# Optimization experiments

Hardware: AMD Instinct MI355X
Metric: run time of the kernel (lower is better)

Reference implementation:

```python
import jax, jax.numpy as jnp
import numpy as np

E = 512        # embed_dim == AutoNCP output_size (motor neurons)
UNITS = 1024   # ncp_units (inter + command + motor)
B = 64         # batch
T = 1024       # sequence length
LN_EPS = 1e-5
SPARSITY = 0.5  # AutoNCP default sparsity_level


def _ncp_sizes():
    rem = UNITS - E
    n_cmd = max(int(0.4 * rem), 1)
    n_inter = rem - n_cmd
    return n_inter, n_cmd, E


def _fanout_mask(rng, n_src, n_dst, fanout):
    # each source neuron connects to `fanout` random targets (NCP-style wiring)
    m = np.zeros((n_src, n_dst), np.float32)
    idx = np.argsort(rng.random((n_src, n_dst)), axis=1)[:, :fanout]
    m[np.arange(n_src)[:, None], idx] = 1.0
    return m


def setup_inputs() -> dict:
    key = jax.random.key(0)
    rng = np.random.default_rng(22222)
    n_inter, n_cmd, n_motor = _ncp_sizes()
    density = 1.0 - SPARSITY
    sensory_fanout = max(int(n_inter * density), 1)
    inter_fanout = max(int(n_cmd * density), 1)
    motor_fanin = max(int(n_cmd * density), 1)
    m0 = _fanout_mask(rng, E, n_inter, sensory_fanout)        # sensory -> inter
    m1 = _fanout_mask(rng, n_inter, n_cmd, inter_fanout)      # inter -> command
    m2 = _fanout_mask(rng, n_motor, n_cmd, motor_fanin).T     # command -> motor (fanin per motor)

    def full_mask(m_in, h):
        # WiredCfCCell: concat ones for the recurrent (hidden) part, then transpose
        # -> mask shape [h, in + h], matching Linear weight [h, in + h]
        return jnp.asarray(np.concatenate([m_in, np.ones((h, h), np.float32)], axis=0).T)

    masks = [full_mask(m0, n_inter), full_mask(m1, n_cmd), full_mask(m2, n_motor)]
    ins = [E, n_inter, n_cmd]
    hs = [n_inter, n_cmd, n_motor]
    d = {}
    ks = jax.random.split(key, 32)
    ki = 0
    for l in range(3):
        fan_in = ins[l] + hs[l]
        scale = float(1.0 / np.sqrt(fan_in))
        for nm in ["ff1", "ff2", "ta", "tb"]:
            d[f"w_{nm}_{l}"] = jax.random.uniform(ks[ki], (hs[l], fan_in), jnp.float32, -scale, scale)
            ki += 1
            d[f"b_{nm}_{l}"] = jnp.zeros((hs[l],), jnp.float32)
        d[f"mask_{l}"] = masks[l]
    d["x"] = jax.random.normal(ks[ki], (B, T, E), jnp.float32)
    d["h0"] = jnp.zeros((B, UNITS), jnp.float32)
    d["ln_gamma"] = jnp.ones((E,), jnp.float32)
    d["ln_beta"] = jnp.zeros((E,), jnp.float32)
    return d


def _cell(z, w1, b1, w2, b2, wa, ba, wb, bb, m):
    # CfCCell (default mode, no backbone), ts = 1.0; sparsity mask on ff1/ff2 only
    ff1 = jnp.tanh(z @ (w1 * m).T + b1)
    ff2 = jnp.tanh(z @ (w2 * m).T + b2)
    t = jax.nn.sigmoid(z @ wa.T + ba + (z @ wb.T + bb))  # sigmoid(t_a * 1.0 + t_b)
    return ff1 * (1.0 - t) + t * ff2


def reference(x, h0, ln_gamma, ln_beta,
              w_ff1_0, b_ff1_0, w_ff2_0, b_ff2_0, w_ta_0, b_ta_0, w_tb_0, b_tb_0, mask_0,
              w_ff1_1, b_ff1_1, w_ff2_1, b_ff2_1, w_ta_1, b_ta_1, w_tb_1, b_tb_1, mask_1,
              w_ff1_2, b_ff1_2, w_ff2_2, b_ff2_2, w_ta_2, b_ta_2, w_tb_2, b_tb_2, mask_2):
    n_inter, n_cmd, _ = _ncp_sizes()
    # LayerNorm over embed_dim
    mu = jnp.mean(x, axis=-1, keepdims=True)
    var = jnp.mean(jnp.square(x - mu), axis=-1, keepdims=True)
    xn = (x - mu) * jax.lax.rsqrt(var + LN_EPS) * ln_gamma + ln_beta
    p0 = (w_ff1_0, b_ff1_0, w_ff2_0, b_ff2_0, w_ta_0, b_ta_0, w_tb_0, b_tb_0, mask_0)
    p1 = (w_ff1_1, b_ff1_1, w_ff2_1, b_ff2_1, w_ta_1, b_ta_1, w_tb_1, b_tb_1, mask_1)
    p2 = (w_ff1_2, b_ff1_2, w_ff2_2, b_ff2_2, w_ta_2, b_ta_2, w_tb_2, b_tb_2, mask_2)

    def step(h, xt):
        h_i, h_c, h_m = jnp.split(h, [n_inter, n_inter + n_cmd], axis=1)
        hi = _cell(jnp.concatenate([xt, h_i], axis=1), *p0)   # inter layer
        hc = _cell(jnp.concatenate([hi, h_c], axis=1), *p1)   # command layer
        hm = _cell(jnp.concatenate([hc, h_m], axis=1), *p2)   # motor layer (block output)
        return jnp.concatenate([hi, hc, hm], axis=1), hm

    h_final, ys = jax.lax.scan(step, h0, jnp.swapaxes(xn, 0, 1))
    y = jnp.swapaxes(ys, 0, 1)  # [B, T, E]; dropout is identity in eval mode
    return y, h_final
```

## Files before the change

### kernel.cpp

```cpp
#include <hip/hip_runtime.h>

typedef __attribute__((ext_vector_type(8))) short short8;
typedef __attribute__((ext_vector_type(4))) float f32x4;
typedef unsigned short ushort_t;
typedef unsigned long long u64_t;

#define T_STEPS 1024
#define NWG 132
#define NWG_MT 33


#define PACK0 0
#define PACK1 1064960
#define PACK2 1517568

#define HI_P (64*320)
#define HC_P (64*224)
#define HM_P (64*512)

#define WS_BAR   0
#define WS_MU    16384
#define WS_RSTD  278528
#define WS_HI    540672
#define WS_HC    622592
#define WS_HM    679936
#define WS_PACK  811008

__device__ __forceinline__ ushort_t f2bf(float f) {
  union { float f; unsigned u; } un; un.f = f;
  unsigned r = (un.u + 0x7fffu + ((un.u >> 16) & 1u)) >> 16;
  return (ushort_t)r;
}

__device__ __forceinline__ void st2(ushort_t* p, ushort_t v) {
  __hip_atomic_store(p, v, __ATOMIC_RELAXED, __HIP_MEMORY_SCOPE_SYSTEM);
}
__device__ __forceinline__ u64_t ld8(const ushort_t* p) {
  return __hip_atomic_load((const u64_t*)p, __ATOMIC_RELAXED, __HIP_MEMORY_SCOPE_SYSTEM);
}
__device__ __forceinline__ unsigned ldf(const unsigned* p) {
  return __hip_atomic_load(p, __ATOMIC_RELAXED, __HIP_MEMORY_SCOPE_SYSTEM);
}
__device__ __forceinline__ void stf(unsigned* p, unsigned v) {
  __hip_atomic_store(p, v, __ATOMIC_RELAXED, __HIP_MEMORY_SCOPE_SYSTEM);
}

__global__ __launch_bounds__(256) void ln_stats(const float* __restrict__ x,
                                                float* __restrict__ mu,
                                                float* __restrict__ rstd) {
  const int row = blockIdx.x * 4 + (threadIdx.x >> 6);
  const int lane = threadIdx.x & 63;
  const float* xr = x + (size_t)row * 512;
  float4 v0 = *(const float4*)(xr + lane * 8);
  float4 v1 = *(const float4*)(xr + lane * 8 + 4);
  float s = v0.x + v0.y + v0.z + v0.w + v1.x + v1.y + v1.z + v1.w;
  float q = v0.x*v0.x + v0.y*v0.y + v0.z*v0.z + v0.w*v0.w
          + v1.x*v1.x + v1.y*v1.y + v1.z*v1.z + v1.w*v1.w;
  for (int m = 1; m <= 32; m <<= 1) {
    s += __shfl_xor(s, m, 64);
    q += __shfl_xor(q, m, 64);
  }
  if (lane == 0) {
    float mean = s * (1.f / 512.f);
    float var = q * (1.f / 512.f) - mean * mean;
    mu[row] = mean;
    rstd[row] = rsqrtf(var + 1e-5f);
  }
}

__global__ void init_h(const float* __restrict__ h0,
                       ushort_t* hi, ushort_t* hc, ushort_t* hm) {
  int i = blockIdx.x * 256 + threadIdx.x;
  if (i >= 64 * 1056) return;
  int b = i / 1056, c = i % 1056;
  if (c < 320) {
    ushort_t v = (c < 308) ? f2bf(h0[b * 1024 + c]) : 0;
    st2(hi + b * 320 + c, v); st2(hi + HI_P + b * 320 + c, v);
  } else if (c < 544) {
    int col = c - 320;
    ushort_t v = (col < 204) ? f2bf(h0[b * 1024 + 308 + col]) : 0;
    st2(hc + b * 224 + col, v); st2(hc + HC_P + b * 224 + col, v);
  } else {
    int col = c - 544;
    ushort_t v = f2bf(h0[b * 1024 + 512 + col]);
    st2(hm + b * 512 + col, v); st2(hm + HM_P + b * 512 + col, v);
  }
}

struct PackP {
  const float* w[12];
  const float* msk[3];
  ushort_t* pack;
};

__global__ __launch_bounds__(256) void ncp_pack(PackP P) {
  int u = blockIdx.x * 256 + threadIdx.x;
  int layer, rem, KB, K, H, s0p, s0l, s1l;
  size_t base;
  if (u < 133120)      { layer = 0; rem = u;          KB = 26; K = 820; H = 308; s0p = 512; s0l = 512; s1l = 308; base = PACK0; }
  else if (u < 189696) { layer = 1; rem = u - 133120; KB = 17; K = 512; H = 204; s0p = 320; s0l = 308; s1l = 204; base = PACK1; }
  else if (u < 378112) { layer = 2; rem = u - 189696; KB = 23; K = 716; H = 512; s0p = 224; s0l = 204; s1l = 512; base = PACK2; }
  else return;
  const int lane = rem & 63;
  const int mat = (rem >> 6) & 3;
  const int kb = (rem >> 8) % KB;
  const int nt = (rem >> 8) / KB;
  const float* W = P.w[layer * 4 + mat];
  const float* M = (mat < 2) ? P.msk[layer] : nullptr;
  const int n = nt * 16 + (lane & 15);
  const int kbase = kb * 32 + ((lane >> 4) << 3);
  ushort_t* dst = P.pack + base + (size_t)rem * 8;
#pragma unroll
  for (int j = 0; j < 8; ++j) {
    const int kp = kbase + j;
    int ko;
    if (kp < s0p) ko = (kp < s0l) ? kp : -1;
    else { const int ks = kp - s0p; ko = (ks < s1l) ? (s0l + ks) : -1; }
    float v = 0.f;
    if (n < H && ko >= 0) {
      v = W[(size_t)n * K + ko];
      if (M) v *= M[(size_t)n * K + ko];
    }
    dst[j] = f2bf(v);
  }
}

struct MainP {
  const float* x;
  const float* gamma;
  const float* beta;
  const float* bias[12];
  const float* mu;
  const float* rstd;
  ushort_t* hi;
  ushort_t* hc;
  ushort_t* hm;
  const ushort_t* pack;
  unsigned* bar;
  float* y;
  float* hfin;
};

#define MAXKB 13

template<int KBT>
__device__ __forceinline__ void load_w(const ushort_t* __restrict__ bp, int lane,
                                       short8 (*w)[4]) {
#pragma unroll
  for (int kb = 0; kb < KBT; ++kb) {
    const ushort_t* q = bp + (size_t)kb * 2048 + lane * 8;
    w[kb][0] = *(const short8*)(q);
    w[kb][1] = *(const short8*)(q + 512);
    w[kb][2] = *(const short8*)(q + 1024);
    w[kb][3] = *(const short8*)(q + 1536);
  }
}

template<int KBT>
__device__ __forceinline__ void span_reg(const short8 (*w)[4],
                                         const ushort_t* __restrict__ lds, int lane,
                                         f32x4& a0, f32x4& a1, f32x4& a2, f32x4& a3) {
#pragma unroll
  for (int kb = 0; kb < KBT; ++kb) {
    short8 av = *(const short8*)(lds + (size_t)(kb * 64 + lane) * 8);
    a0 = __builtin_amdgcn_mfma_f32_16x16x32_bf16(av, w[kb][0], a0, 0, 0, 0);
    a1 = __builtin_amdgcn_mfma_f32_16x16x32_bf16(av, w[kb][1], a1, 0, 0, 0);
    a2 = __builtin_amdgcn_mfma_f32_16x16x32_bf16(av, w[kb][2], a2, 0, 0, 0);
    a3 = __builtin_amdgcn_mfma_f32_16x16x32_bf16(av, w[kb][3], a3, 0, 0, 0);
  }
}

template<int H, int STP>
__device__ __forceinline__ void epi_h(const f32x4* A, int nt, int lane, int mtile,
                                      const float* __restrict__ bp1, const float* __restrict__ bp2,
                                      const float* __restrict__ bpa, const float* __restrict__ bpb,
                                      ushort_t* __restrict__ hout, float* vk) {
  const int n = nt * 16 + (lane & 15);
  const int r0 = (lane >> 4) << 2;
#pragma unroll
  for (int j = 0; j < 4; ++j) vk[j] = 0.f;
  if (n < H) {
    float c1 = bp1[n], c2 = bp2[n], ca = bpa[n], cb = bpb[n];
#pragma unroll
    for (int j = 0; j < 4; ++j) {
      int brow = mtile * 16 + r0 + j;
      float sg = 1.f / (1.f + __expf(-(A[2][j] + ca + A[3][j] + cb)));
      float f1 = 1.f - 2.f / (1.f + __expf(2.f * (A[0][j] + c1)));
      float f2 = 1.f - 2.f / (1.f + __expf(2.f * (A[1][j] + c2)));
      float v = f1 * (1.f - sg) + sg * f2;
      vk[j] = v;
      st2(hout + (size_t)brow * STP + n, f2bf(v));
    }
  }
}

template<int S1, int ST1, int S2, int ST2>
__device__ __forceinline__ void stage2(ushort_t* __restrict__ r1, const ushort_t* __restrict__ h1,
                                       ushort_t* __restrict__ r2, const ushort_t* __restrict__ h2,
                                       int tid) {
  constexpr int U1 = S1 * 2, U2 = S2 * 2;
  constexpr int I1 = (U1 + 255) / 256;
  constexpr int I2 = (U2 + 255) / 256;
  u64_t a[I1];
  u64_t b[I2 > 0 ? I2 : 1];
#pragma unroll
  for (int i = 0; i < I1; ++i) {
    const int u = tid + i * 256;
    if ((U1 & 255) == 0 || u < U1) {
      const int slot = u >> 1;
      a[i] = ld8(h1 + (slot & 15) * ST1 + (slot >> 6) * 32 + ((slot >> 4) & 3) * 8 + (u & 1) * 4);
    }
  }
  if constexpr (S2 > 0) {
#pragma unroll
    for (int i = 0; i < I2; ++i) {
      const int u = tid + i * 256;
      if ((U2 & 255) == 0 || u < U2) {
        const int slot = u >> 1;
        b[i] = ld8(h2 + (slot & 15) * ST2 + (slot >> 6) * 32 + ((slot >> 4) & 3) * 8 + (u & 1) * 4);
      }
    }
  }
#pragma unroll
  for (int i = 0; i < I1; ++i) {
    const int u = tid + i * 256;
    if ((U1 & 255) == 0 || u < U1) *(u64_t*)(r1 + (size_t)u * 4) = a[i];
  }
  if constexpr (S2 > 0) {
#pragma unroll
    for (int i = 0; i < I2; ++i) {
      const int u = tid + i * 256;
      if ((U2 & 255) == 0 || u < U2) *(u64_t*)(r2 + (size_t)u * 4) = b[i];
    }
  }
}

__device__ __forceinline__ void stage_xn(ushort_t* __restrict__ XN, const MainP& P,
                                         int mtile, int tid, int t) {
#pragma unroll
  for (int i = 0; i < 4; ++i) {
    const int s = tid + i * 256;
    const int ln = s & 63;
    const int brow = mtile * 16 + (ln & 15);
    const int kbase = (s >> 6) * 32 + ((ln >> 4) << 3);
    const float muv = P.mu[brow * T_STEPS + t];
    const float rsv = P.rstd[brow * T_STEPS + t];
    const f32x4* xr = (const f32x4*)(P.x + ((size_t)brow * T_STEPS + t) * 512 + kbase);
    f32x4 xv0 = __builtin_nontemporal_load(xr);
    f32x4 xv1 = __builtin_nontemporal_load(xr + 1);
    const f32x4 g0 = *(const f32x4*)(P.gamma + kbase);
    const f32x4 g1 = *(const f32x4*)(P.gamma + kbase + 4);
    const f32x4 b0 = *(const f32x4*)(P.beta + kbase);
    const f32x4 b1 = *(const f32x4*)(P.beta + kbase + 4);
    short8 w;
#pragma unroll
    for (int j = 0; j < 4; ++j) w[j] = f2bf((xv0[j] - muv) * rsv * g0[j] + b0[j]);
#pragma unroll
    for (int j = 0; j < 4; ++j) w[4 + j] = f2bf((xv1[j] - muv) * rsv * g1[j] + b1[j]);
    *(short8*)(XN + (size_t)s * 8) = w;
  }
}

__device__ __forceinline__ void poll_wf(const unsigned* wfbase, int a, int cnt,
                                        int lane, unsigned need) {
  const unsigned* p = wfbase + (a + (lane < cnt ? lane : 0)) * 16;
  const bool act = lane < cnt;
  for (;;) {
    unsigned v = act ? ldf(p) : 0xFFFFFFFFu;
    if (__all((int)(v >= need))) break;
    __builtin_amdgcn_s_sleep(1);
  }
}

__global__ __launch_bounds__(256, 1) void ncp_main(MainP P) {
  const int tid = threadIdx.x;
  const int lane = tid & 63;
  const int wv = tid >> 6;
  const int role = wv & 1;
  const int tslot = wv >> 1;
  const int wg = blockIdx.x;
  const int mt = wg / NWG_MT;
  const int r  = wg % NWG_MT;

  __shared__ __align__(16) ushort_t Alds[2688 * 8];
  __shared__ __align__(16) f32x4 pacc[2][256];

  unsigned* wf = P.bar + mt * 1024;
  int wa, wb;
  int ma, mb;
  if (r < 10)      { wa = 0;  wb = 10; ma = 10; mb = 17; }
  else if (r < 17) { wa = 0;  wb = 17; ma = 17; mb = 33; }
  else             { wa = 10; wb = 33; ma = 0;  mb = 0;  }

  int nt = 0;
  bool valid = true;
  if (r < 10)      nt = r * 2 + tslot;
  else if (r < 17) { nt = (r - 10) * 2 + tslot; valid = (nt < 13); }
  else             nt = (r - 17) * 2 + tslot;

  short8 wreg[MAXKB][4];
  if (valid) {
    if (r < 10) {
      const ushort_t* bp = P.pack + PACK0 + (size_t)nt * 26 * 2048 + (role ? 13 : 0) * 2048;
      load_w<13>(bp, lane, wreg);
    } else if (r < 17) {
      const ushort_t* bp = P.pack + PACK1 + (size_t)nt * 17 * 2048;
      if (role == 0) load_w<9>(bp, lane, wreg);
      else           load_w<8>(bp + 9 * 2048, lane, wreg);
    } else {
      const ushort_t* bp = P.pack + PACK2 + (size_t)nt * 23 * 2048;
      if (role == 0) load_w<12>(bp, lane, wreg);
      else           load_w<11>(bp + 12 * 2048, lane, wreg);
    }
  }

  if (r < 10) stage_xn(Alds, P, mt, tid, 0);

  for (int s = 0; s < T_STEPS + 2; ++s) {
    if (wv == 0) poll_wf(wf, wa, wb - wa, lane, (unsigned)s);
    __syncthreads();

    int tstep = 0;
    bool on = false;
    if (r < 10)      { tstep = s;     on = (s < T_STEPS); }
    else if (r < 17) { tstep = s - 1; on = (s >= 1 && s <= T_STEPS) && valid; }
    else             { tstep = s - 2; on = (s >= 2); }
    const bool last = (tstep == T_STEPS - 1);

    if (r < 10) {
      if (s < T_STEPS)
        stage2<640, 320, 0, 0>(Alds + 2048 * 8,
                               P.hi + (((s - 1) & 1) * 64 + mt * 16) * 320,
                               nullptr, nullptr, tid);
    } else if (r < 17) {
      if (s >= 1 && s <= T_STEPS)
        stage2<640, 320, 448, 224>(Alds, P.hi + (((s - 1) & 1) * 64 + mt * 16) * 320,
                                   Alds + 640 * 8,
                                   P.hc + (((s - 2) & 1) * 64 + mt * 16) * 224, tid);
    } else {
      if (s >= 2)
        stage2<448, 224, 1024, 512>(Alds, P.hc + (((s - 2) & 1) * 64 + mt * 16) * 224,
                                    Alds + 448 * 8,
                                    P.hm + (((s - 3) & 1) * 64 + mt * 16) * 512, tid);
    }
    __syncthreads();

    f32x4 A[4];
#pragma unroll
    for (int j = 0; j < 4; ++j) A[j] = {0.f, 0.f, 0.f, 0.f};
    if (on) {
      if (r < 10) {
        const ushort_t* XNc = Alds + (s & 1) * (1024 * 8);
        const ushort_t* HIl = Alds + 2048 * 8;
        if (role == 0) span_reg<13>(wreg, XNc, lane, A[0], A[1], A[2], A[3]);
        else { span_reg<3>(wreg, XNc + 13 * 512, lane, A[0], A[1], A[2], A[3]);
               span_reg<10>(wreg + 3, HIl, lane, A[0], A[1], A[2], A[3]); }
      } else if (r < 17) {
        const ushort_t* HIr = Alds;
        const ushort_t* HCr = Alds + 640 * 8;
        if (role == 0) span_reg<9>(wreg, HIr, lane, A[0], A[1], A[2], A[3]);
        else { span_reg<1>(wreg, HIr + 9 * 512, lane, A[0], A[1], A[2], A[3]);
               span_reg<7>(wreg + 1, HCr, lane, A[0], A[1], A[2], A[3]); }
      } else {
        const ushort_t* HCr = Alds;
        const ushort_t* HMr = Alds + 448 * 8;
        if (role == 0) { span_reg<7>(wreg, HCr, lane, A[0], A[1], A[2], A[3]);
                         span_reg<5>(wreg + 7, HMr, lane, A[0], A[1], A[2], A[3]); }
        else           span_reg<11>(wreg, HMr + 5 * 512, lane, A[0], A[1], A[2], A[3]);
      }
      if (role == 1) {
#pragma unroll
        for (int j = 0; j < 4; ++j) pacc[tslot][j * 64 + lane] = A[j];
      }
    }
    __syncthreads();

    float vk[4];
    if (on && role == 0) {
      if (mb > ma) poll_wf(wf, ma, mb - ma, lane, (unsigned)s);
#pragma unroll
      for (int j = 0; j < 4; ++j) {
        f32x4 p = pacc[tslot][j * 64 + lane];
        A[j][0] += p[0]; A[j][1] += p[1]; A[j][2] += p[2]; A[j][3] += p[3];
      }
      if (r < 10)
        epi_h<308, 320>(A, nt, lane, mt, P.bias[0], P.bias[1], P.bias[2], P.bias[3],
                        P.hi + (tstep & 1) * HI_P, vk);
      else if (r < 17)
        epi_h<204, 224>(A, nt, lane, mt, P.bias[4], P.bias[5], P.bias[6], P.bias[7],
                        P.hc + (tstep & 1) * HC_P, vk);
      else
        epi_h<512, 512>(A, nt, lane, mt, P.bias[8], P.bias[9], P.bias[10], P.bias[11],
                        P.hm + (tstep & 1) * HM_P, vk);
    }
    asm volatile("s_waitcnt vmcnt(0)" ::: "memory");
    __syncthreads();
    if (tid == 0) stf(wf + r * 16, (unsigned)(s + 1));

    if (on && role == 0) {
      const int n_ = nt * 16 + (lane & 15);
      const int r0 = (lane >> 4) << 2;
      const int H_ = (r < 10) ? 308 : ((r < 17) ? 204 : 512);
      const int hoff = (r < 10) ? 0 : ((r < 17) ? 308 : 512);
      if (n_ < H_) {
#pragma unroll
        for (int j = 0; j < 4; ++j) {
          const int brow = mt * 16 + r0 + j;
          if (r >= 17)
            __builtin_nontemporal_store(vk[j], &P.y[((size_t)brow * T_STEPS + tstep) * 512 + n_]);
          if (last)
            __builtin_nontemporal_store(vk[j], &P.hfin[brow * 1024 + hoff + n_]);
        }
      }
    }

    if (r < 10 && s + 1 < T_STEPS)
      stage_xn(Alds + ((s + 1) & 1) * (1024 * 8), P, mt, tid, s + 1);
  }
}

extern "C" void kernel_launch(void* const* d_in, const int* in_sizes, int n_in,
                              void* d_out, int out_size, void* d_ws, size_t ws_size,
                              hipStream_t stream) {
  const float* x     = (const float*)d_in[27];
  const float* h0    = (const float*)d_in[28];
  const float* gamma = (const float*)d_in[29];
  const float* beta  = (const float*)d_in[30];

  char* ws = (char*)d_ws;
  unsigned* bar = (unsigned*)(ws + WS_BAR);
  float* mu   = (float*)(ws + WS_MU);
  float* rstd = (float*)(ws + WS_RSTD);
  ushort_t* hi = (ushort_t*)(ws + WS_HI);
  ushort_t* hc = (ushort_t*)(ws + WS_HC);
  ushort_t* hm = (ushort_t*)(ws + WS_HM);
  ushort_t* pack = (ushort_t*)(ws + WS_PACK);

  float* y = (float*)d_out;
  float* hfin = y + (size_t)64 * 1024 * 512;

  hipMemsetAsync(bar, 0, 16384, stream);

  ln_stats<<<dim3(16384), dim3(256), 0, stream>>>(x, mu, rstd);
  init_h<<<dim3(264), dim3(256), 0, stream>>>(h0, hi, hc, hm);

  PackP pp;
  for (int l = 0; l < 3; ++l) {
    for (int m = 0; m < 4; ++m) pp.w[l * 4 + m] = (const float*)d_in[l * 9 + 2 * m];
    pp.msk[l] = (const float*)d_in[l * 9 + 8];
  }
  pp.pack = pack;
  ncp_pack<<<dim3(1477), dim3(256), 0, stream>>>(pp);

  MainP mp;
  mp.x = x; mp.gamma = gamma; mp.beta = beta;
  for (int l = 0; l < 3; ++l)
    for (int m = 0; m < 4; ++m) mp.bias[l * 4 + m] = (const float*)d_in[l * 9 + 2 * m + 1];
  mp.mu = mu; mp.rstd = rstd;
  mp.hi = hi; mp.hc = hc; mp.hm = hm;
  mp.pack = pack; mp.bar = bar;
  mp.y = y; mp.hfin = hfin;
  ncp_main<<<dim3(NWG), dim3(256), 0, stream>>>(mp);
}
```

Measured before the change: 6.730 ms.

## Quad-buffer hidden states to drop the mid-step WAR poll

Hidden-state buffers for each layer go from double to quadruple buffering, and the workspace offsets grow to fit. With the extra slack, the write-after-read poll that each layer ran before its epilogue is removed. It is replaced by a looser readiness check (step s-2) folded into the single poll at the top of each step. This takes one global flag-polling round off every timestep's critical path, at the cost of more workspace memory and a reliance on the new lag bound being enough for correctness.

```diff
diff --git a/kernel.cpp b/kernel.cpp
--- a/kernel.cpp
+++ b/kernel.cpp
@@ -22,9 +22,9 @@
 #define WS_MU    16384
 #define WS_RSTD  278528
 #define WS_HI    540672
-#define WS_HC    622592
-#define WS_HM    679936
-#define WS_PACK  811008
+#define WS_HC    704512
+#define WS_HM    819200
+#define WS_PACK  1081344
 
 __device__ __forceinline__ ushort_t f2bf(float f) {
   union { float f; unsigned u; } un; un.f = f;
@@ -75,15 +75,18 @@
   int b = i / 1056, c = i % 1056;
   if (c < 320) {
     ushort_t v = (c < 308) ? f2bf(h0[b * 1024 + c]) : 0;
-    st2(hi + b * 320 + c, v); st2(hi + HI_P + b * 320 + c, v);
+#pragma unroll
+    for (int p = 0; p < 4; ++p) st2(hi + p * HI_P + b * 320 + c, v);
   } else if (c < 544) {
     int col = c - 320;
     ushort_t v = (col < 204) ? f2bf(h0[b * 1024 + 308 + col]) : 0;
-    st2(hc + b * 224 + col, v); st2(hc + HC_P + b * 224 + col, v);
+#pragma unroll
+    for (int p = 0; p < 4; ++p) st2(hc + p * HC_P + b * 224 + col, v);
   } else {
     int col = c - 544;
     ushort_t v = f2bf(h0[b * 1024 + 512 + col]);
-    st2(hm + b * 512 + col, v); st2(hm + HM_P + b * 512 + col, v);
+#pragma unroll
+    for (int p = 0; p < 4; ++p) st2(hm + p * HM_P + b * 512 + col, v);
   }
 }
 
@@ -261,10 +264,14 @@
   }
 }
 
-__device__ __forceinline__ void poll_wf(const unsigned* wfbase, int a, int cnt,
-                                        int lane, unsigned need) {
-  const unsigned* p = wfbase + (a + (lane < cnt ? lane : 0)) * 16;
-  const bool act = lane < cnt;
+__device__ __forceinline__ void poll2(const unsigned* wfbase, int lane,
+                                      int a1, int c1, unsigned need1,
+                                      int a2, int c2, unsigned need2) {
+  const unsigned* p = wfbase;
+  unsigned need = 0;
+  bool act = false;
+  if (lane < c1)           { p = wfbase + (a1 + lane) * 16;        need = need1; act = true; }
+  else if (lane < c1 + c2) { p = wfbase + (a2 + lane - c1) * 16;   need = need2; act = true; }
   for (;;) {
     unsigned v = act ? ldf(p) : 0xFFFFFFFFu;
     if (__all((int)(v >= need))) break;
@@ -286,11 +293,10 @@
   __shared__ __align__(16) f32x4 pacc[2][256];
 
   unsigned* wf = P.bar + mt * 1024;
-  int wa, wb;
-  int ma, mb;
-  if (r < 10)      { wa = 0;  wb = 10; ma = 10; mb = 17; }
-  else if (r < 17) { wa = 0;  wb = 17; ma = 17; mb = 33; }
-  else             { wa = 10; wb = 33; ma = 0;  mb = 0;  }
+  int a1, c1, a2, c2;
+  if (r < 10)      { a1 = 0;  c1 = 10; a2 = 10; c2 = 7;  }
+  else if (r < 17) { a1 = 0;  c1 = 17; a2 = 17; c2 = 16; }
+  else             { a1 = 10; c1 = 23; a2 = 0;  c2 = 0;  }
 
   int nt = 0;
   bool valid = true;
@@ -317,7 +323,11 @@
   if (r < 10) stage_xn(Alds, P, mt, tid, 0);
 
   for (int s = 0; s < T_STEPS + 2; ++s) {
-    if (wv == 0) poll_wf(wf, wa, wb - wa, lane, (unsigned)s);
+    if (wv == 0) {
+      const unsigned needA = (unsigned)s;
+      const unsigned needB = (s >= 2) ? (unsigned)(s - 2) : 0u;
+      poll2(wf, lane, a1, c1, needA, a2, c2, needB);
+    }
     __syncthreads();
 
     int tstep = 0;
@@ -330,18 +340,18 @@
     if (r < 10) {
       if (s < T_STEPS)
         stage2<640, 320, 0, 0>(Alds + 2048 * 8,
-                               P.hi + (((s - 1) & 1) * 64 + mt * 16) * 320,
+                               P.hi + (((s - 1) & 3) * 64 + mt * 16) * 320,
                                nullptr, nullptr, tid);
     } else if (r < 17) {
       if (s >= 1 && s <= T_STEPS)
-        stage2<640, 320, 448, 224>(Alds, P.hi + (((s - 1) & 1) * 64 + mt * 16) * 320,
+        stage2<640, 320, 448, 224>(Alds, P.hi + (((s - 1) & 3) * 64 + mt * 16) * 320,
                                    Alds + 640 * 8,
-                                   P.hc + (((s - 2) & 1) * 64 + mt * 16) * 224, tid);
+                                   P.hc + (((s - 2) & 3) * 64 + mt * 16) * 224, tid);
     } else {
       if (s >= 2)
-        stage2<448, 224, 1024, 512>(Alds, P.hc + (((s - 2) & 1) * 64 + mt * 16) * 224,
+        stage2<448, 224, 1024, 512>(Alds, P.hc + (((s - 2) & 3) * 64 + mt * 16) * 224,
                                     Alds + 448 * 8,
-                                    P.hm + (((s - 3) & 1) * 64 + mt * 16) * 512, tid);
+                                    P.hm + (((s - 3) & 3) * 64 + mt * 16) * 512, tid);
     }
     __syncthreads();
 
@@ -377,7 +387,6 @@
 
     float vk[4];
     if (on && role == 0) {
-      if (mb > ma) poll_wf(wf, ma, mb - ma, lane, (unsigned)s);
 #pragma unroll
       for (int j = 0; j < 4; ++j) {
         f32x4 p = pacc[tslot][j * 64 + lane];
@@ -385,13 +394,13 @@
       }
       if (r < 10)
         epi_h<308, 320>(A, nt, lane, mt, P.bias[0], P.bias[1], P.bias[2], P.bias[3],
-                        P.hi + (tstep & 1) * HI_P, vk);
+                        P.hi + (tstep & 3) * HI_P, vk);
       else if (r < 17)
         epi_h<204, 224>(A, nt, lane, mt, P.bias[4], P.bias[5], P.bias[6], P.bias[7],
-                        P.hc + (tstep & 1) * HC_P, vk);
+                        P.hc + (tstep & 3) * HC_P, vk);
       else
         epi_h<512, 512>(A, nt, lane, mt, P.bias[8], P.bias[9], P.bias[10], P.bias[11],
-                        P.hm + (tstep & 1) * HM_P, vk);
+                        P.hm + (tstep & 3) * HM_P, vk);
     }
     asm volatile("s_waitcnt vmcnt(0)" ::: "memory");
     __syncthreads();
```

After: 6.650 ms. No clear change (-1.2%).
